# Optimization experiments

Hardware: AMD Instinct MI355X
Metric: run time of the kernel (lower is better)

## Reference

```python
import jax, jax.numpy as jnp
import numpy as np

IN, OUT, RANK = 4096, 4096, 8
ALPHA = 8.0

def _quantize_int8(x):
    # row-wise symmetric int8 quantization (matches torch _quantize_int8)
    scale = jnp.max(jnp.abs(x), axis=1) / 127.0              # [rows]
    q = jnp.round(x / jnp.clip(scale, 1e-12)[:, None]).astype(jnp.int8)
    return q, scale


def setup_inputs() -> dict:
    key = jax.random.key(0)
    k_x, k_w, k_a, k_b = jax.random.split(key, 4)
    x = jax.random.normal(k_x, (8192, IN), dtype=jnp.float32)
    # simulate quantizing a pretrained fp32 weight [OUT, IN]
    w = jax.random.normal(k_w, (OUT, IN), dtype=jnp.float32) * 0.02
    w_scale = jnp.max(jnp.abs(w), axis=1) / 127.0
    weight_i8 = jnp.round(w / jnp.clip(w_scale, 1e-12)[:, None]).astype(jnp.int8)
    weight_scale = w_scale.astype(jnp.float32)               # [OUT]
    # LoRA params (lora_b random instead of zeros so output is nontrivial)
    lora_a = jax.random.normal(k_a, (RANK, IN), dtype=jnp.float32) * (1.0 / np.sqrt(IN))
    lora_b = jax.random.normal(k_b, (OUT, RANK), dtype=jnp.float32) * 0.02
    return {"x": x, "weight_i8": weight_i8, "weight_scale": weight_scale,
            "lora_a": lora_a, "lora_b": lora_b}


def reference(x, weight_i8, weight_scale, lora_a, lora_b):
    # quantize_act=True path: int8 activation quant + int8 GEMM (int32 accum) + dequant
    x_i8, x_scale = _quantize_int8(x)                         # [T, IN] int8, [T]
    out_i32 = jnp.matmul(x_i8, weight_i8.T, preferred_element_type=jnp.int32)  # [T, OUT]
    out = out_i32.astype(jnp.float32) * x_scale[:, None] * weight_scale[None, :]
    # LoRA low-rank add: x @ A^T @ B^T * (alpha / rank)
    out = out + (x @ lora_a.T) @ lora_b.T * (ALPHA / RANK)
    return out
```

## Files before the change

### kernel.cpp

```cpp
#include <hip/hip_runtime.h>
#include <stdint.h>

#define T_DIM   8192
#define IN_DIM  4096
#define OUT_DIM 4096
#define RANK    8

typedef int v4i __attribute__((ext_vector_type(4)));

__device__ __forceinline__ void async_copy16(const void* g, void* l) {
  __builtin_amdgcn_global_load_lds(
      (const __attribute__((address_space(1))) void*)g,
      (__attribute__((address_space(3))) void*)l, 16, 0, 0);
}

__global__ __launch_bounds__(256) void pack_w(
    const int* __restrict__ w32, int8_t* __restrict__ w8)
{
  const int idx = blockIdx.x * 256 + threadIdx.x;
  const int4 v = ((const int4*)w32)[idx];
  char4 q;
  q.x = (signed char)v.x; q.y = (signed char)v.y;
  q.z = (signed char)v.z; q.w = (signed char)v.w;
  ((char4*)w8)[idx] = q;
}

#define Q_ROWS 8
#define Q_THREADS 512

__global__ __launch_bounds__(Q_THREADS) void quant_lora_a(
    const float* __restrict__ x,
    const float* __restrict__ lora_a,
    int8_t* __restrict__ x_i8,
    float* __restrict__ x_scale,
    float* __restrict__ xa)
{
  const int tid = threadIdx.x;
  const int row0 = blockIdx.x * Q_ROWS;

  float4 av[RANK][2];
#pragma unroll
  for (int r = 0; r < RANK; ++r)
#pragma unroll
    for (int c = 0; c < 2; ++c)
      av[r][c] = ((const float4*)(lora_a + (size_t)r * IN_DIM))[c * 512 + tid];

  __shared__ float red[8][12];

  for (int rr = 0; rr < Q_ROWS; ++rr) {
    const int row = row0 + rr;
    const float4* xr = (const float4*)(x + (size_t)row * IN_DIM);
    float4 xv[2];
#pragma unroll
    for (int c = 0; c < 2; ++c) xv[c] = xr[c * 512 + tid];

    float am = 0.f;
#pragma unroll
    for (int c = 0; c < 2; ++c)
      am = fmaxf(am, fmaxf(fmaxf(fabsf(xv[c].x), fabsf(xv[c].y)),
                           fmaxf(fabsf(xv[c].z), fabsf(xv[c].w))));
    float dots[RANK];
#pragma unroll
    for (int r = 0; r < RANK; ++r) {
      float s = 0.f;
#pragma unroll
      for (int c = 0; c < 2; ++c)
        s += xv[c].x * av[r][c].x + xv[c].y * av[r][c].y +
             xv[c].z * av[r][c].z + xv[c].w * av[r][c].w;
      dots[r] = s;
    }
#pragma unroll
    for (int off = 32; off > 0; off >>= 1) {
      am = fmaxf(am, __shfl_xor(am, off, 64));
#pragma unroll
      for (int r = 0; r < RANK; ++r) dots[r] += __shfl_xor(dots[r], off, 64);
    }
    const int wave = tid >> 6;
    if ((tid & 63) == 0) {
      red[wave][0] = am;
#pragma unroll
      for (int r = 0; r < RANK; ++r) red[wave][1 + r] = dots[r];
    }
    __syncthreads();
    float amax = 0.f;
#pragma unroll
    for (int w = 0; w < 8; ++w) amax = fmaxf(amax, red[w][0]);
    const float scale = amax * (1.0f / 127.0f);
    const float inv = 1.0f / fmaxf(scale, 1e-12f);

    char4* qout = (char4*)(x_i8 + (size_t)row * IN_DIM);
#pragma unroll
    for (int c = 0; c < 2; ++c) {
      char4 q;
      q.x = (signed char)(int)rintf(xv[c].x * inv);
      q.y = (signed char)(int)rintf(xv[c].y * inv);
      q.z = (signed char)(int)rintf(xv[c].z * inv);
      q.w = (signed char)(int)rintf(xv[c].w * inv);
      qout[c * 512 + tid] = q;
    }
    if (tid == 0) x_scale[row] = scale;
    if (tid < RANK) {
      float d = 0.f;
#pragma unroll
      for (int w = 0; w < 8; ++w) d += red[w][1 + tid];
      xa[(size_t)row * RANK + tid] = d;
    }
    __syncthreads();
  }
}

__global__ __launch_bounds__(256) void int8_gemm_lora(
    const int8_t* __restrict__ A,
    const int8_t* __restrict__ B,
    const float* __restrict__ x_scale,
    const float* __restrict__ w_scale,
    const float* __restrict__ xa,
    const float* __restrict__ lora_b,
    float* __restrict__ out)
{
  __shared__ __align__(16) int8_t As[128 * 64];
  __shared__ __align__(16) int8_t Bs[128 * 64];
  __shared__ float xs_s[128];
  __shared__ float ws_s[128];
  __shared__ __align__(16) float xa_s[128 * RANK];
  __shared__ __align__(16) float lb_s[128 * RANK];

  const int tid = threadIdx.x;
  const int bx = blockIdx.x & 31;
  const int by = blockIdx.x >> 5;
  const size_t arow0 = (size_t)by * 128;
  const size_t brow0 = (size_t)bx * 128;

  if (tid < 128) xs_s[tid] = x_scale[arow0 + tid];
  else           ws_s[tid - 128] = w_scale[brow0 + (tid - 128)];
  ((float4*)xa_s)[tid] = ((const float4*)(xa + arow0 * RANK))[tid];
  ((float4*)lb_s)[tid] = ((const float4*)(lora_b + brow0 * RANK))[tid];

  v4i acc[4][4];
  const v4i vzero = {0, 0, 0, 0};
#pragma unroll
  for (int i = 0; i < 4; ++i)
#pragma unroll
    for (int j = 0; j < 4; ++j) acc[i][j] = vzero;

  const int lane = tid & 63;
  const int wave = tid >> 6;
  const int wr = wave >> 1, wc = wave & 1;
  const int quad = lane >> 4, m16 = lane & 15;

  const int8_t* a_frag_base = As + ((wr * 64 + m16) * 64 + quad * 16);
  const int8_t* b_frag_base = Bs + ((wc * 64 + m16) * 64 + quad * 16);

  const int off0 = tid * 16;
  const int r0 = tid >> 2;
  const int c0 = (tid & 3) * 16;
  const int8_t* a_src = A + (arow0 + (size_t)r0) * IN_DIM + c0;
  const int8_t* b_src = B + (brow0 + (size_t)r0) * IN_DIM + c0;

  for (int k0 = 0; k0 < IN_DIM; k0 += 64) {
    async_copy16(a_src + k0,                         As + off0);
    async_copy16(a_src + (size_t)64 * IN_DIM + k0,   As + 4096 + off0);
    async_copy16(b_src + k0,                         Bs + off0);
    async_copy16(b_src + (size_t)64 * IN_DIM + k0,   Bs + 4096 + off0);
    __syncthreads();

    v4i aF[4], bF[4];
#pragma unroll
    for (int i = 0; i < 4; ++i) aF[i] = *(const v4i*)(a_frag_base + i * 16 * 64);
#pragma unroll
    for (int j = 0; j < 4; ++j) bF[j] = *(const v4i*)(b_frag_base + j * 16 * 64);
#pragma unroll
    for (int i = 0; i < 4; ++i)
#pragma unroll
      for (int j = 0; j < 4; ++j)
        acc[i][j] = __builtin_amdgcn_mfma_i32_16x16x64_i8(aF[i], bF[j], acc[i][j], 0, 0, 0);
    __syncthreads();
  }

  float wscv[4];
  float4 lb0[4], lb1[4];
  int cols[4];
#pragma unroll
  for (int j = 0; j < 4; ++j) {
    const int c = wc * 64 + j * 16 + m16;
    cols[j] = c;
    wscv[j] = ws_s[c];
    lb0[j] = *(const float4*)(lb_s + c * RANK);
    lb1[j] = *(const float4*)(lb_s + c * RANK + 4);
  }
#pragma unroll
  for (int i = 0; i < 4; ++i) {
#pragma unroll
    for (int reg = 0; reg < 4; ++reg) {
      const int r = wr * 64 + i * 16 + quad * 4 + reg;
      const float xsc = xs_s[r];
      const float4 xa0 = *(const float4*)(xa_s + r * RANK);
      const float4 xa1 = *(const float4*)(xa_s + r * RANK + 4);
      float* orow = out + (arow0 + (size_t)r) * OUT_DIM + brow0;
#pragma unroll
      for (int j = 0; j < 4; ++j) {
        float v = (float)acc[i][j][reg] * xsc * wscv[j];
        v += xa0.x * lb0[j].x + xa0.y * lb0[j].y + xa0.z * lb0[j].z + xa0.w * lb0[j].w +
             xa1.x * lb1[j].x + xa1.y * lb1[j].y + xa1.z * lb1[j].z + xa1.w * lb1[j].w;
        orow[cols[j]] = v;
      }
    }
  }
}

extern "C" void kernel_launch(void* const* d_in, const int* in_sizes, int n_in,
                              void* d_out, int out_size, void* d_ws, size_t ws_size,
                              hipStream_t stream) {
  const float*  x        = (const float*)d_in[0];
  const int*    w_i32    = (const int*)d_in[1];
  const float*  w_scale  = (const float*)d_in[2];
  const float*  lora_a   = (const float*)d_in[3];
  const float*  lora_b   = (const float*)d_in[4];
  float* out = (float*)d_out;

  int8_t* x_i8   = (int8_t*)d_ws;
  int8_t* w8     = x_i8 + (size_t)T_DIM * IN_DIM;
  float* x_scale = (float*)(w8 + (size_t)OUT_DIM * IN_DIM);
  float* xa      = x_scale + T_DIM;

  pack_w<<<(OUT_DIM * IN_DIM / 4) / 256, 256, 0, stream>>>(w_i32, w8);
  quant_lora_a<<<T_DIM / Q_ROWS, Q_THREADS, 0, stream>>>(x, lora_a, x_i8, x_scale, xa);
  int8_gemm_lora<<<(T_DIM / 128) * (OUT_DIM / 128), 256, 0, stream>>>(
      x_i8, w8, x_scale, w_scale, xa, lora_b, out);
}
```

Measured before the change: 462.7 us.

## Use 32x32 int8 MFMA in GEMM and compute LoRA-A projection via bf16 MFMA

The main GEMM switches from 16x16x64 to 32x32x32 int8 MFMA tiles, with the epilogue row mapping updated to match. Activation quantization is split into a per-row kernel. The x@A^T LoRA projection moves to a separate bf16 MFMA kernel that reads the quantized int8 activations and rescales by x_scale. The lora_a conversion to bf16 is fused into the weight-pack launch. Computing xa from quantized x instead of fp32 x changes the numerics, adds an extra launch, and rereads x_i8 from memory.

```diff
diff --git a/kernel.cpp b/kernel.cpp
--- a/kernel.cpp
+++ b/kernel.cpp
@@ -6,7 +6,10 @@
 #define OUT_DIM 4096
 #define RANK    8
 
-typedef int v4i __attribute__((ext_vector_type(4)));
+typedef int   v4i  __attribute__((ext_vector_type(4)));
+typedef int   v16i __attribute__((ext_vector_type(16)));
+typedef short v8s  __attribute__((ext_vector_type(8)));
+typedef float v4f  __attribute__((ext_vector_type(4)));
 
 __device__ __forceinline__ void async_copy16(const void* g, void* l) {
   __builtin_amdgcn_global_load_lds(
@@ -14,98 +17,106 @@
       (__attribute__((address_space(3))) void*)l, 16, 0, 0);
 }
 
-__global__ __launch_bounds__(256) void pack_w(
-    const int* __restrict__ w32, int8_t* __restrict__ w8)
-{
-  const int idx = blockIdx.x * 256 + threadIdx.x;
-  const int4 v = ((const int4*)w32)[idx];
-  char4 q;
-  q.x = (signed char)v.x; q.y = (signed char)v.y;
-  q.z = (signed char)v.z; q.w = (signed char)v.w;
-  ((char4*)w8)[idx] = q;
-}
-
-#define Q_ROWS 8
-#define Q_THREADS 512
-
-__global__ __launch_bounds__(Q_THREADS) void quant_lora_a(
-    const float* __restrict__ x,
-    const float* __restrict__ lora_a,
-    int8_t* __restrict__ x_i8,
-    float* __restrict__ x_scale,
+__device__ __forceinline__ unsigned short f2bf_rne(float f) {
+  unsigned int x = __builtin_bit_cast(unsigned int, f);
+  return (unsigned short)((x + 0x7fffu + ((x >> 16) & 1u)) >> 16);
+}
+
+#define PACKW_BLOCKS 16384
+#define PACKA_BLOCKS 256
+
+__global__ __launch_bounds__(256) void pack_inputs(
+    const int* __restrict__ w32, const float* __restrict__ lora_a,
+    int8_t* __restrict__ w8, unsigned short* __restrict__ a_bf)
+{
+  const int b = blockIdx.x;
+  if (b < PACKW_BLOCKS) {
+    const int idx = b * 256 + threadIdx.x;
+    const int4 v = ((const int4*)w32)[idx];
+    char4 q;
+    q.x = (signed char)v.x; q.y = (signed char)v.y;
+    q.z = (signed char)v.z; q.w = (signed char)v.w;
+    ((char4*)w8)[idx] = q;
+  } else {
+    const int idx = (b - PACKW_BLOCKS) * 256 + threadIdx.x;
+    const int r = idx >> 12;
+    const int k = idx & (IN_DIM - 1);
+    const float v = (r < RANK) ? lora_a[(size_t)r * IN_DIM + k] : 0.f;
+    a_bf[idx] = f2bf_rne(v);
+  }
+}
+
+__global__ __launch_bounds__(256) void quant_row(
+    const float* __restrict__ x, int8_t* __restrict__ x_i8,
+    float* __restrict__ x_scale)
+{
+  const int row = blockIdx.x;
+  const int tid = threadIdx.x;
+  const float4* xr = (const float4*)(x + (size_t)row * IN_DIM);
+  float4 xv[4];
+#pragma unroll
+  for (int c = 0; c < 4; ++c) xv[c] = xr[c * 256 + tid];
+
+  float am = 0.f;
+#pragma unroll
+  for (int c = 0; c < 4; ++c)
+    am = fmaxf(am, fmaxf(fmaxf(fabsf(xv[c].x), fabsf(xv[c].y)),
+                         fmaxf(fabsf(xv[c].z), fabsf(xv[c].w))));
+#pragma unroll
+  for (int off = 32; off > 0; off >>= 1)
+    am = fmaxf(am, __shfl_xor(am, off, 64));
+
+  __shared__ float red[4];
+  if ((tid & 63) == 0) red[tid >> 6] = am;
+  __syncthreads();
+  const float amax = fmaxf(fmaxf(red[0], red[1]), fmaxf(red[2], red[3]));
+  const float scale = amax * (1.0f / 127.0f);
+  const float inv = 1.0f / fmaxf(scale, 1e-12f);
+
+  char4* qout = (char4*)(x_i8 + (size_t)row * IN_DIM);
+#pragma unroll
+  for (int c = 0; c < 4; ++c) {
+    char4 q;
+    q.x = (signed char)(int)rintf(xv[c].x * inv);
+    q.y = (signed char)(int)rintf(xv[c].y * inv);
+    q.z = (signed char)(int)rintf(xv[c].z * inv);
+    q.w = (signed char)(int)rintf(xv[c].w * inv);
+    qout[c * 256 + tid] = q;
+  }
+  if (tid == 0) x_scale[row] = scale;
+}
+
+__global__ __launch_bounds__(256) void xa_mfma(
+    const int8_t* __restrict__ x_i8, const float* __restrict__ x_scale,
+    const unsigned short* __restrict__ a_bf,
     float* __restrict__ xa)
 {
   const int tid = threadIdx.x;
-  const int row0 = blockIdx.x * Q_ROWS;
-
-  float4 av[RANK][2];
-#pragma unroll
-  for (int r = 0; r < RANK; ++r)
-#pragma unroll
-    for (int c = 0; c < 2; ++c)
-      av[r][c] = ((const float4*)(lora_a + (size_t)r * IN_DIM))[c * 512 + tid];
-
-  __shared__ float red[8][12];
-
-  for (int rr = 0; rr < Q_ROWS; ++rr) {
-    const int row = row0 + rr;
-    const float4* xr = (const float4*)(x + (size_t)row * IN_DIM);
-    float4 xv[2];
-#pragma unroll
-    for (int c = 0; c < 2; ++c) xv[c] = xr[c * 512 + tid];
-
-    float am = 0.f;
-#pragma unroll
-    for (int c = 0; c < 2; ++c)
-      am = fmaxf(am, fmaxf(fmaxf(fabsf(xv[c].x), fabsf(xv[c].y)),
-                           fmaxf(fabsf(xv[c].z), fabsf(xv[c].w))));
-    float dots[RANK];
-#pragma unroll
-    for (int r = 0; r < RANK; ++r) {
-      float s = 0.f;
-#pragma unroll
-      for (int c = 0; c < 2; ++c)
-        s += xv[c].x * av[r][c].x + xv[c].y * av[r][c].y +
-             xv[c].z * av[r][c].z + xv[c].w * av[r][c].w;
-      dots[r] = s;
+  const int lane = tid & 63, wave = tid >> 6;
+  const int row0 = blockIdx.x * 64 + wave * 16;
+  const int m16 = lane & 15, quad = lane >> 4;
+
+  v4f acc = {0.f, 0.f, 0.f, 0.f};
+  const int8_t* arow = x_i8 + (size_t)(row0 + m16) * IN_DIM + quad * 8;
+  const unsigned short* brow = a_bf + (size_t)m16 * IN_DIM + quad * 8;
+
+  for (int k0 = 0; k0 < IN_DIM; k0 += 32) {
+    const uint2 a8 = *(const uint2*)(arow + k0);
+    v8s aF;
+#pragma unroll
+    for (int j = 0; j < 8; ++j) {
+      const unsigned int word = (j < 4) ? a8.x : a8.y;
+      const signed char sc = (signed char)((word >> ((j & 3) * 8)) & 0xff);
+      aF[j] = (short)(__builtin_bit_cast(unsigned int, (float)(int)sc) >> 16);
     }
-#pragma unroll
-    for (int off = 32; off > 0; off >>= 1) {
-      am = fmaxf(am, __shfl_xor(am, off, 64));
-#pragma unroll
-      for (int r = 0; r < RANK; ++r) dots[r] += __shfl_xor(dots[r], off, 64);
-    }
-    const int wave = tid >> 6;
-    if ((tid & 63) == 0) {
-      red[wave][0] = am;
-#pragma unroll
-      for (int r = 0; r < RANK; ++r) red[wave][1 + r] = dots[r];
-    }
-    __syncthreads();
-    float amax = 0.f;
-#pragma unroll
-    for (int w = 0; w < 8; ++w) amax = fmaxf(amax, red[w][0]);
-    const float scale = amax * (1.0f / 127.0f);
-    const float inv = 1.0f / fmaxf(scale, 1e-12f);
-
-    char4* qout = (char4*)(x_i8 + (size_t)row * IN_DIM);
-#pragma unroll
-    for (int c = 0; c < 2; ++c) {
-      char4 q;
-      q.x = (signed char)(int)rintf(xv[c].x * inv);
-      q.y = (signed char)(int)rintf(xv[c].y * inv);
-      q.z = (signed char)(int)rintf(xv[c].z * inv);
-      q.w = (signed char)(int)rintf(xv[c].w * inv);
-      qout[c * 512 + tid] = q;
-    }
-    if (tid == 0) x_scale[row] = scale;
-    if (tid < RANK) {
-      float d = 0.f;
-#pragma unroll
-      for (int w = 0; w < 8; ++w) d += red[w][1 + tid];
-      xa[(size_t)row * RANK + tid] = d;
-    }
-    __syncthreads();
+    const v8s bF = *(const v8s*)(brow + k0);
+    acc = __builtin_amdgcn_mfma_f32_16x16x32_bf16(aF, bF, acc, 0, 0, 0);
+  }
+  const int r = row0 + quad * 4;
+  if (m16 < RANK) {
+#pragma unroll
+    for (int reg = 0; reg < 4; ++reg)
+      xa[(size_t)(r + reg) * RANK + m16] = acc[reg] * x_scale[r + reg];
   }
 }
 
@@ -136,20 +147,21 @@
   ((float4*)xa_s)[tid] = ((const float4*)(xa + arow0 * RANK))[tid];
   ((float4*)lb_s)[tid] = ((const float4*)(lora_b + brow0 * RANK))[tid];
 
-  v4i acc[4][4];
-  const v4i vzero = {0, 0, 0, 0};
-#pragma unroll
-  for (int i = 0; i < 4; ++i)
-#pragma unroll
-    for (int j = 0; j < 4; ++j) acc[i][j] = vzero;
+  v16i acc[2][2];
+#pragma unroll
+  for (int i = 0; i < 2; ++i)
+#pragma unroll
+    for (int j = 0; j < 2; ++j)
+#pragma unroll
+      for (int e = 0; e < 16; ++e) acc[i][j][e] = 0;
 
   const int lane = tid & 63;
   const int wave = tid >> 6;
   const int wr = wave >> 1, wc = wave & 1;
-  const int quad = lane >> 4, m16 = lane & 15;
-
-  const int8_t* a_frag_base = As + ((wr * 64 + m16) * 64 + quad * 16);
-  const int8_t* b_frag_base = Bs + ((wc * 64 + m16) * 64 + quad * 16);
+  const int l31 = lane & 31, lh = lane >> 5;
+
+  const int8_t* a_frag_base = As + (wr * 64 + l31) * 64 + lh * 16;
+  const int8_t* b_frag_base = Bs + (wc * 64 + l31) * 64 + lh * 16;
 
   const int off0 = tid * 16;
   const int r0 = tid >> 2;
@@ -158,51 +170,59 @@
   const int8_t* b_src = B + (brow0 + (size_t)r0) * IN_DIM + c0;
 
   for (int k0 = 0; k0 < IN_DIM; k0 += 64) {
-    async_copy16(a_src + k0,                         As + off0);
-    async_copy16(a_src + (size_t)64 * IN_DIM + k0,   As + 4096 + off0);
-    async_copy16(b_src + k0,                         Bs + off0);
-    async_copy16(b_src + (size_t)64 * IN_DIM + k0,   Bs + 4096 + off0);
+    async_copy16(a_src + k0,                       As + off0);
+    async_copy16(a_src + (size_t)64 * IN_DIM + k0, As + 4096 + off0);
+    async_copy16(b_src + k0,                       Bs + off0);
+    async_copy16(b_src + (size_t)64 * IN_DIM + k0, Bs + 4096 + off0);
     __syncthreads();
 
-    v4i aF[4], bF[4];
-#pragma unroll
-    for (int i = 0; i < 4; ++i) aF[i] = *(const v4i*)(a_frag_base + i * 16 * 64);
-#pragma unroll
-    for (int j = 0; j < 4; ++j) bF[j] = *(const v4i*)(b_frag_base + j * 16 * 64);
-#pragma unroll
-    for (int i = 0; i < 4; ++i)
-#pragma unroll
-      for (int j = 0; j < 4; ++j)
-        acc[i][j] = __builtin_amdgcn_mfma_i32_16x16x64_i8(aF[i], bF[j], acc[i][j], 0, 0, 0);
+    v4i aF[2][2], bF[2][2];
+#pragma unroll
+    for (int ks = 0; ks < 2; ++ks) {
+#pragma unroll
+      for (int i = 0; i < 2; ++i) {
+        aF[ks][i] = *(const v4i*)(a_frag_base + i * 32 * 64 + ks * 32);
+        bF[ks][i] = *(const v4i*)(b_frag_base + i * 32 * 64 + ks * 32);
+      }
+    }
+#pragma unroll
+    for (int ks = 0; ks < 2; ++ks)
+#pragma unroll
+      for (int i = 0; i < 2; ++i)
+#pragma unroll
+        for (int j = 0; j < 2; ++j)
+          acc[i][j] = __builtin_amdgcn_mfma_i32_32x32x32_i8(
+              aF[ks][i], bF[ks][j], acc[i][j], 0, 0, 0);
     __syncthreads();
   }
 
-  float wscv[4];
-  float4 lb0[4], lb1[4];
-  int cols[4];
-#pragma unroll
-  for (int j = 0; j < 4; ++j) {
-    const int c = wc * 64 + j * 16 + m16;
-    cols[j] = c;
+  float wscv[2];
+  float4 lb0v[2], lb1v[2];
+  int colv[2];
+#pragma unroll
+  for (int j = 0; j < 2; ++j) {
+    const int c = wc * 64 + j * 32 + l31;
+    colv[j] = c;
     wscv[j] = ws_s[c];
-    lb0[j] = *(const float4*)(lb_s + c * RANK);
-    lb1[j] = *(const float4*)(lb_s + c * RANK + 4);
-  }
-#pragma unroll
-  for (int i = 0; i < 4; ++i) {
-#pragma unroll
-    for (int reg = 0; reg < 4; ++reg) {
-      const int r = wr * 64 + i * 16 + quad * 4 + reg;
+    lb0v[j] = *(const float4*)(lb_s + c * RANK);
+    lb1v[j] = *(const float4*)(lb_s + c * RANK + 4);
+  }
+#pragma unroll
+  for (int i = 0; i < 2; ++i) {
+#pragma unroll
+    for (int reg = 0; reg < 16; ++reg) {
+      const int rit = (reg & 3) + 8 * (reg >> 2) + 4 * lh;
+      const int r = wr * 64 + i * 32 + rit;
       const float xsc = xs_s[r];
       const float4 xa0 = *(const float4*)(xa_s + r * RANK);
       const float4 xa1 = *(const float4*)(xa_s + r * RANK + 4);
       float* orow = out + (arow0 + (size_t)r) * OUT_DIM + brow0;
 #pragma unroll
-      for (int j = 0; j < 4; ++j) {
+      for (int j = 0; j < 2; ++j) {
         float v = (float)acc[i][j][reg] * xsc * wscv[j];
-        v += xa0.x * lb0[j].x + xa0.y * lb0[j].y + xa0.z * lb0[j].z + xa0.w * lb0[j].w +
-             xa1.x * lb1[j].x + xa1.y * lb1[j].y + xa1.z * lb1[j].z + xa1.w * lb1[j].w;
-        orow[cols[j]] = v;
+        v += xa0.x * lb0v[j].x + xa0.y * lb0v[j].y + xa0.z * lb0v[j].z + xa0.w * lb0v[j].w +
+             xa1.x * lb1v[j].x + xa1.y * lb1v[j].y + xa1.z * lb1v[j].z + xa1.w * lb1v[j].w;
+        orow[colv[j]] = v;
       }
     }
   }
@@ -211,20 +231,22 @@
 extern "C" void kernel_launch(void* const* d_in, const int* in_sizes, int n_in,
                               void* d_out, int out_size, void* d_ws, size_t ws_size,
                               hipStream_t stream) {
-  const float*  x        = (const float*)d_in[0];
-  const int*    w_i32    = (const int*)d_in[1];
-  const float*  w_scale  = (const float*)d_in[2];
-  const float*  lora_a   = (const float*)d_in[3];
-  const float*  lora_b   = (const float*)d_in[4];
+  const float* x       = (const float*)d_in[0];
+  const int*   w_i32   = (const int*)d_in[1];
+  const float* w_scale = (const float*)d_in[2];
+  const float* lora_a  = (const float*)d_in[3];
+  const float* lora_b  = (const float*)d_in[4];
   float* out = (float*)d_out;
 
-  int8_t* x_i8   = (int8_t*)d_ws;
-  int8_t* w8     = x_i8 + (size_t)T_DIM * IN_DIM;
-  float* x_scale = (float*)(w8 + (size_t)OUT_DIM * IN_DIM);
+  int8_t* x_i8 = (int8_t*)d_ws;
+  int8_t* w8   = x_i8 + (size_t)T_DIM * IN_DIM;
+  unsigned short* a_bf = (unsigned short*)(w8 + (size_t)OUT_DIM * IN_DIM);
+  float* x_scale = (float*)(a_bf + 16 * IN_DIM);
   float* xa      = x_scale + T_DIM;
 
-  pack_w<<<(OUT_DIM * IN_DIM / 4) / 256, 256, 0, stream>>>(w_i32, w8);
-  quant_lora_a<<<T_DIM / Q_ROWS, Q_THREADS, 0, stream>>>(x, lora_a, x_i8, x_scale, xa);
+  pack_inputs<<<PACKW_BLOCKS + PACKA_BLOCKS, 256, 0, stream>>>(w_i32, lora_a, w8, a_bf);
+  quant_row<<<T_DIM, 256, 0, stream>>>(x, x_i8, x_scale);
+  xa_mfma<<<T_DIM / 64, 256, 0, stream>>>(x_i8, x_scale, a_bf, xa);
   int8_gemm_lora<<<(T_DIM / 128) * (OUT_DIM / 128), 256, 0, stream>>>(
       x_i8, w8, x_scale, w_scale, xa, lora_b, out);
 }
```

Result: slower. 488.9 us (+5.6%).
